# Kernel tuning notes

Hardware: AMD Instinct MI355X
Metric: run time of the kernel (lower is better)

The kernel has to match this reference:

```python
import jax, jax.numpy as jnp
import numpy as np

VOCAB, EMB, HID = 32000, 512, 1024
B, T = 16, 128


def setup_inputs() -> dict:
    key = jax.random.key(0)
    ks = jax.random.split(key, 12)
    bound = 1.0 / np.sqrt(HID)
    u = lambda k, shape: jax.random.uniform(k, shape, jnp.float32, -bound, bound)
    return {
        "sentence": jax.random.randint(ks[0], (B, T), 0, VOCAB),
        "emb": jax.random.normal(ks[1], (VOCAB, EMB), jnp.float32),
        "W_i": u(ks[2], (EMB + HID, HID)), "b_i": u(ks[3], (HID,)),
        "W_f": u(ks[4], (EMB + HID, HID)), "b_f": u(ks[5], (HID,)),
        "W_o": u(ks[6], (EMB + HID, HID)), "b_o": u(ks[7], (HID,)),
        "W_c": u(ks[8], (EMB + HID, HID)), "b_c": u(ks[9], (HID,)),
        "W_hq": u(ks[10], (HID, VOCAB)), "b_q": u(ks[11], (VOCAB,)),
    }


def reference(sentence, emb, W_i, b_i, W_f, b_f, W_o, b_o, W_c, b_c, W_hq, b_q):
    # [B,T,E] -> [T,B,E]
    x = jnp.swapaxes(emb[sentence], 0, 1)
    # Fuse the 4 gate matmuls into one concatenated-weight matmul (same math).
    W = jnp.concatenate([W_i, W_f, W_o, W_c], axis=1)  # [E+H, 4H]
    b = jnp.concatenate([b_i, b_f, b_o, b_c])          # [4H]
    h0 = jnp.zeros((x.shape[1], HID), x.dtype)

    def step(carry, xt):
        h, c = carry
        z = jnp.concatenate([xt, h], axis=1) @ W + b   # [B,4H]
        i, f, o, g = jnp.split(z, 4, axis=1)
        i, f, o = jax.nn.sigmoid(i), jax.nn.sigmoid(f), jax.nn.sigmoid(o)
        c = f * c + i * jnp.tanh(g)
        h = o * jnp.tanh(c)
        return (h, c), h

    _, hs = jax.lax.scan(step, (h0, h0), x)            # [T,B,H]
    out = jnp.einsum('tbh,hv->tbv', hs, W_hq) + b_q    # [T,B,V]
    return jnp.transpose(out, (1, 2, 0))               # [B,V,T] as in torch permute(1,2,0)
```

## Files before the change

kernel.cpp:

```cpp
#include <hip/hip_runtime.h>
#include <math.h>

typedef float f32x4 __attribute__((ext_vector_type(4)));
typedef short bf16x8 __attribute__((ext_vector_type(8)));
typedef unsigned short u16;
typedef unsigned int u32;
typedef unsigned long long u64;

#define FLAG_STRIDE 16
#define ACQ_BASE    8192
#define EPOCH_BASE  8448
#define QCNT_BASE   8512
#define TCNT_BASE   8528
#define FLAG_WORDS  ((TCNT_BASE + 1) * FLAG_STRIDE)
#define NTILE       125

__device__ __forceinline__ u16 f2bf(float f) {
    union { float f; unsigned u; } x; x.f = f;
    unsigned r = x.u + 0x7fff + ((x.u >> 16) & 1);
    return (u16)(r >> 16);
}

__device__ __forceinline__ void gload_lds16(const u16* g, u16* l) {
    __builtin_amdgcn_global_load_lds(
        (const __attribute__((address_space(1))) void*)g,
        (__attribute__((address_space(3))) void*)l, 16, 0, 0);
}

__global__ __launch_bounds__(256) void prep(
    const int* __restrict__ sent, const float* __restrict__ emb, u16* __restrict__ xb,
    const float* __restrict__ bi, const float* __restrict__ bf_,
    const float* __restrict__ bo, const float* __restrict__ bc, float* __restrict__ b4,
    const float* __restrict__ Wi, const float* __restrict__ Wf,
    const float* __restrict__ Wo, const float* __restrict__ Wc, u16* __restrict__ wxt) {
    __shared__ float tile[32][33];
    const int bx = blockIdx.x, tid = threadIdx.x;
    if (bx < 1024) {
        int row = bx * 2 + (tid >> 7);
        int t = row >> 4, b = row & 15;
        int idx = sent[b * 128 + t];
        float4 v = ((const float4*)(emb + (size_t)idx * 512))[tid & 127];
        ushort4 s = { f2bf(v.x), f2bf(v.y), f2bf(v.z), f2bf(v.w) };
        ((ushort4*)(xb + (size_t)row * 512))[tid & 127] = s;
        return;
    }
    if (bx < 1040) {
        int i = (bx - 1024) * 256 + tid;
        const float* p = (i < 1024) ? bi : (i < 2048) ? bf_ : (i < 3072) ? bo : bc;
        b4[i] = p[i & 1023];
        return;
    }
    int q = bx - 1040, g = q >> 9, r = q & 511;
    const float* in = (g == 0) ? Wi : (g == 1) ? Wf : (g == 2) ? Wo : Wc;
    u16* out = wxt + (size_t)g * 1024 * 512;
    int rt = (r >> 5) * 32, ct = (r & 31) * 32;
    {
        int rr = tid >> 3, cq = (tid & 7) * 4;
        float4 v = *(const float4*)(in + (size_t)(rt + rr) * 1024 + ct + cq);
        tile[rr][cq] = v.x; tile[rr][cq + 1] = v.y; tile[rr][cq + 2] = v.z; tile[rr][cq + 3] = v.w;
        __syncthreads();
        int c = tid >> 3, rq = (tid & 7) * 4;
        ushort4 s = { f2bf(tile[rq][c]), f2bf(tile[rq + 1][c]),
                      f2bf(tile[rq + 2][c]), f2bf(tile[rq + 3][c]) };
        *(ushort4*)(out + (size_t)(ct + c) * 512 + rt + rq) = s;
    }
}

__global__ __launch_bounds__(256) void gemm_xz(
    const u16* __restrict__ A, const u16* __restrict__ Bt,
    const float* __restrict__ bias, float* __restrict__ C) {
    const int tid = threadIdx.x;
    const int l = tid & 63, w = tid >> 6;
    const int wr = w >> 1, wc = w & 1;
    const int m0 = blockIdx.x * 128, n0 = blockIdx.y * 128;
    const int K = 512;
    __shared__ __align__(16) u16 As[128 * 64];
    __shared__ __align__(16) u16 Bs[128 * 64];
    f32x4 acc[4][4];
    f32x4 zz = { 0.f, 0.f, 0.f, 0.f };
#pragma unroll
    for (int i = 0; i < 4; i++)
#pragma unroll
        for (int j = 0; j < 4; j++) acc[i][j] = zz;
    for (int kt = 0; kt < (K >> 6); ++kt) {
        __syncthreads();
#pragma unroll
        for (int i = 0; i < 4; i++) {
            int cbase = i * 256 + w * 64;
            int c = cbase + l, row = c >> 3, kc = c & 7;
            gload_lds16(A + (size_t)(m0 + row) * K + kt * 64 + kc * 8, As + (size_t)cbase * 8);
            gload_lds16(Bt + (size_t)(n0 + row) * K + kt * 64 + kc * 8, Bs + (size_t)cbase * 8);
        }
        __syncthreads();
#pragma unroll
        for (int kk = 0; kk < 2; kk++) {
            bf16x8 af[4], bfv[4];
#pragma unroll
            for (int mi = 0; mi < 4; mi++)
                af[mi] = *(const bf16x8*)(As + (wr * 64 + mi * 16 + (l & 15)) * 64 + kk * 32 + (l >> 4) * 8);
#pragma unroll
            for (int ni = 0; ni < 4; ni++)
                bfv[ni] = *(const bf16x8*)(Bs + (wc * 64 + ni * 16 + (l & 15)) * 64 + kk * 32 + (l >> 4) * 8);
#pragma unroll
            for (int mi = 0; mi < 4; mi++)
#pragma unroll
                for (int ni = 0; ni < 4; ni++)
                    acc[mi][ni] = __builtin_amdgcn_mfma_f32_16x16x32_bf16(af[mi], bfv[ni], acc[mi][ni], 0, 0, 0);
        }
    }
    const int lr = l >> 4, lc = l & 15;
#pragma unroll
    for (int ni = 0; ni < 4; ni++) {
        int col = n0 + wc * 64 + ni * 16 + lc;
        float bv = bias[col];
#pragma unroll
        for (int mi = 0; mi < 4; mi++)
#pragma unroll
            for (int r = 0; r < 4; r++) {
                int row = m0 + wr * 64 + mi * 16 + lr * 4 + r;
                C[(size_t)row * 4096 + col] = acc[mi][ni][r] + bv;
            }
    }
}

__global__ __launch_bounds__(512, 2) void lstm_proj(
    u16* __restrict__ hs,
    const float* __restrict__ xz,
    const float* __restrict__ Wi, const float* __restrict__ Wf,
    const float* __restrict__ Wo, const float* __restrict__ Wc,
    u32* __restrict__ flags,
    const float* __restrict__ Whq,
    u16* __restrict__ whqt,
    const float* __restrict__ bq, float* __restrict__ out) {
    __shared__ __align__(16) char smem[98816];
    const int bx = blockIdx.x;
    const int tid = threadIdx.x;
    const int w = tid >> 6, l = tid & 63;

    if (tid == 0)
        __hip_atomic_fetch_add(&flags[(size_t)(ACQ_BASE + (bx & 255)) * FLAG_STRIDE], 0u,
                               __ATOMIC_ACQ_REL, __HIP_MEMORY_SCOPE_AGENT);

    if (bx < 64) {
        u16* hstage = (u16*)smem;
        float (*zlds)[16][17] = (float (*)[16][17])(void*)(smem + 32768);
        u32* lds_cnt = (u32*)(smem + 37632);
        const int j = bx;
        const int row = l & 15, hi = l >> 4;
        if (tid == 0) *lds_cnt = 0;

        bf16x8 wf[32];
        if (w < 4) {
            const float* Wg = (w == 0) ? Wi : (w == 1) ? Wf : (w == 2) ? Wo : Wc;
#pragma unroll
            for (int kk = 0; kk < 32; ++kk)
#pragma unroll
                for (int e = 0; e < 8; ++e)
                    wf[kk][e] = f2bf(Wg[(size_t)(512 + kk * 32 + hi * 8 + e) * 1024 + j * 16 + row]);
        }
        __syncthreads();

        const int b = tid >> 4, hc = tid & 15;
        float cst = 0.f;
        float cz0 = 0.f, cz1 = 0.f, cz2 = 0.f, cz3 = 0.f;
        if (tid < 256) {
            const float* xr0 = xz + (size_t)b * 4096 + j * 16 + hc;
            cz0 = xr0[0]; cz1 = xr0[1024]; cz2 = xr0[2048]; cz3 = xr0[3072];
        }

        for (int t = 0; t < 128; ++t) {
            if (t > 0) {
                const u16* hbase = hs + (size_t)(t - 1) * 16 * 1024;
                {
                    int spins = 0;
                    while (true) {
                        u32 f = 1u;
                        if (l < 8)
                            f = __hip_atomic_load(
                                    &flags[(size_t)((t - 1) * 64 + 8 * w + l) * FLAG_STRIDE],
                                    __ATOMIC_RELAXED, __HIP_MEMORY_SCOPE_SYSTEM);
                        if (__ballot(f != 0u) == ~0ull) break;
                        __builtin_amdgcn_s_sleep(1);
                        if (++spins > (1 << 20)) break;
                    }
                }
#pragma unroll
                for (int q = 0; q < 4; ++q) {
                    int jw0 = 8 * w + 2 * q;
                    gload_lds16(hbase + (size_t)((l & 31) >> 1) * 1024
                                      + (jw0 + (l >> 5)) * 16 + (l & 1) * 8,
                                hstage + (size_t)jw0 * 256);
                }
            }
            float nz0 = 0.f, nz1 = 0.f, nz2 = 0.f, nz3 = 0.f;
            if (t < 127 && tid < 256) {
                const float* xr = xz + (size_t)((t + 1) * 16 + b) * 4096 + j * 16 + hc;
                nz0 = xr[0]; nz1 = xr[1024]; nz2 = xr[2048]; nz3 = xr[3072];
            }
            __syncthreads();
            if (t > 0) {
                if (tid == 0)
                    __hip_atomic_store(&flags[(size_t)(EPOCH_BASE + j) * FLAG_STRIDE], (u32)t,
                                       __ATOMIC_RELAXED, __HIP_MEMORY_SCOPE_SYSTEM);
                if (w < 4) {
                    f32x4 zv = { 0.f, 0.f, 0.f, 0.f };
                    f32x4 ac0 = zv, ac1 = zv, ac2 = zv, ac3 = zv;
#pragma unroll
                    for (int kk = 0; kk < 32; kk += 4) {
#pragma unroll
                        for (int u = 0; u < 4; ++u) {
                            int base = (2 * (kk + u) + (hi >> 1)) * 256 + row * 16 + (hi & 1) * 8;
                            bf16x8 a = *(const bf16x8*)(hstage + base);
                            f32x4& ac = (u == 0) ? ac0 : (u == 1) ? ac1 : (u == 2) ? ac2 : ac3;
                            ac = __builtin_amdgcn_mfma_f32_16x16x32_bf16(a, wf[kk + u], ac, 0, 0, 0);
                        }
                    }
                    f32x4 acc = (ac0 + ac1) + (ac2 + ac3);
#pragma unroll
                    for (int r = 0; r < 4; ++r)
                        zlds[w][hi * 4 + r][row] = acc[r];
                }
            }
            __syncthreads();
            if (tid < 256) {
                float zi = cz0, zf = cz1, zo = cz2, zc = cz3;
                if (t > 0) {
                    zi += zlds[0][b][hc]; zf += zlds[1][b][hc];
                    zo += zlds[2][b][hc]; zc += zlds[3][b][hc];
                }
                float ig = 1.f / (1.f + __expf(-zi));
                float fg = 1.f / (1.f + __expf(-zf));
                float og = 1.f / (1.f + __expf(-zo));
                float gg = tanhf(zc);
                cst = fg * cst + ig * gg;
                float h = og * tanhf(cst);
                float hn = __shfl_xor(h, 1);
                if (!(l & 1)) {
                    unsigned pk = (unsigned)f2bf(h) | ((unsigned)f2bf(hn) << 16);
                    u32* dst = (u32*)hs + (((size_t)(t * 16 + b) * 1024 + j * 16 + hc) >> 1);
                    __hip_atomic_store(dst, pk, __ATOMIC_RELAXED, __HIP_MEMORY_SCOPE_SYSTEM);
                }
                cz0 = nz0; cz1 = nz1; cz2 = nz2; cz3 = nz3;
            }
            if (w < 4) {
                asm volatile("s_waitcnt vmcnt(0)" ::: "memory");
                if (l == 0) {
                    u32 old = atomicAdd(lds_cnt, 1u);
                    if (old == (u32)(4 * t + 3))
                        __hip_atomic_store(&flags[(size_t)(t * 64 + j) * FLAG_STRIDE], 1u,
                                           __ATOMIC_RELAXED, __HIP_MEMORY_SCOPE_SYSTEM);
                }
            }
        }
        if (w == 0) {
            int spins = 0;
            while (true) {
                u32 f = __hip_atomic_load(&flags[(size_t)(127 * 64 + l) * FLAG_STRIDE],
                                          __ATOMIC_RELAXED, __HIP_MEMORY_SCOPE_SYSTEM);
                if (__ballot(f != 0) == ~0ull) break;
                __builtin_amdgcn_s_sleep(1);
                if (++spins > (1 << 20)) break;
            }
            if (l == 0)
                __hip_atomic_store(&flags[(size_t)(EPOCH_BASE + j) * FLAG_STRIDE], 128u,
                                   __ATOMIC_RELAXED, __HIP_MEMORY_SCOPE_SYSTEM);
        }
        return;
    }

    {
        float (*tp)[32][33] = (float (*)[32][33])(void*)smem;
        const int half = tid >> 8, t256 = tid & 255;
        const int r = t256 >> 3, cq = (t256 & 7) * 4;
        const int c = t256 >> 3, rq = (t256 & 7) * 4;
        for (int it = 0; it < 84; ++it) {
            int q = it * 384 + (bx - 64) * 2 + half;
            bool act = q < 32000;
            int rt = 0, ct = 0;
            if (act) { rt = (q / 1000) * 32; ct = (q % 1000) * 32; }
            if (act) {
                float4 v = *(const float4*)(Whq + (size_t)(rt + r) * 32000 + ct + cq);
                tp[half][r][cq] = v.x; tp[half][r][cq + 1] = v.y;
                tp[half][r][cq + 2] = v.z; tp[half][r][cq + 3] = v.w;
            }
            __syncthreads();
            if (act) {
                u64 pk = (u64)f2bf(tp[half][rq][c])
                       | ((u64)f2bf(tp[half][rq + 1][c]) << 16)
                       | ((u64)f2bf(tp[half][rq + 2][c]) << 32)
                       | ((u64)f2bf(tp[half][rq + 3][c]) << 48);
                __hip_atomic_store((u64*)(whqt + (size_t)(ct + c) * 1024 + rt + rq), pk,
                                   __ATOMIC_RELAXED, __HIP_MEMORY_SCOPE_SYSTEM);
            }
            __syncthreads();
        }
        asm volatile("s_waitcnt vmcnt(0)" ::: "memory");
        if (tid == 0)
            __hip_atomic_fetch_add(&flags[(size_t)TCNT_BASE * FLAG_STRIDE], 1u,
                                   __ATOMIC_RELAXED, __HIP_MEMORY_SCOPE_SYSTEM);
    }

    u16* As = (u16*)smem;
    u16* Bs = (u16*)(smem + 32768);
    u32* idx_slot = (u32*)(smem + 98304);
    const int wr = w >> 2, wc = w & 3;
    const int lr = l >> 4, lc = l & 15;

    if (tid == 0)
        *idx_slot = __hip_atomic_fetch_add(&flags[(size_t)QCNT_BASE * FLAG_STRIDE],
                                           1u, __ATOMIC_RELAXED, __HIP_MEMORY_SCOPE_AGENT);
    if (w == 0) {
        int spins = 0;
        while (__hip_atomic_load(&flags[(size_t)TCNT_BASE * FLAG_STRIDE],
                                 __ATOMIC_RELAXED, __HIP_MEMORY_SCOPE_SYSTEM) < 192u) {
            __builtin_amdgcn_s_sleep(8);
            if (++spins > (1 << 20)) break;
        }
    }
    __syncthreads();
    const u32 myIdx = *idx_slot;
    if (myIdx >= NTILE) return;
    const int n0 = (int)myIdx * 256;

    for (int m = 0; m < 16; ++m) {
        if (w == 0) {
            const u32 need = (u32)(8 * m + 8);
            int spins = 0;
            while (__hip_atomic_load(&flags[(size_t)(EPOCH_BASE + (bx & 63)) * FLAG_STRIDE],
                                     __ATOMIC_RELAXED, __HIP_MEMORY_SCOPE_SYSTEM) < need) {
                __builtin_amdgcn_s_sleep(8);
                if (++spins > (1 << 20)) break;
            }
        }
        __syncthreads();

        auto STAGE = [&](int bi, int kt) {
#pragma unroll
            for (int i = 0; i < 2; ++i) {
                int C = i * 512 + tid, r = C >> 3, c = C & 7;
                int sc = c ^ (r & 7);
                int arow = (8 * m + (r & 7)) * 16 + (r >> 3);
                gload_lds16(hs + (size_t)arow * 1024 + kt * 64 + sc * 8,
                            As + (size_t)(bi * 8192 + (i * 512 + w * 64) * 8));
            }
#pragma unroll
            for (int i = 0; i < 4; ++i) {
                int C = i * 512 + tid, r = C >> 3, c = C & 7;
                int sc = c ^ (r & 7);
                gload_lds16(whqt + (size_t)(n0 + r) * 1024 + kt * 64 + sc * 8,
                            Bs + (size_t)(bi * 16384 + (i * 512 + w * 64) * 8));
            }
        };

        f32x4 acc[4][4];
        f32x4 zz = { 0.f, 0.f, 0.f, 0.f };
#pragma unroll
        for (int i = 0; i < 4; i++)
#pragma unroll
            for (int jj = 0; jj < 4; jj++) acc[i][jj] = zz;

        int cur = 0;
        STAGE(0, 0);
        __syncthreads();
        for (int kt = 0; kt < 16; ++kt) {
            if (kt + 1 < 16) STAGE(cur ^ 1, kt + 1);
            const u16* Ab = As + cur * 8192;
            const u16* Bb = Bs + cur * 16384;
#pragma unroll
            for (int kk = 0; kk < 2; ++kk) {
                bf16x8 af[4], bf[4];
#pragma unroll
                for (int mi = 0; mi < 4; ++mi) {
                    int rA = wr * 64 + mi * 16 + lc;
                    int s = (kk * 4 + lr) ^ (rA & 7);
                    af[mi] = *(const bf16x8*)(Ab + rA * 64 + s * 8);
                }
#pragma unroll
                for (int ni = 0; ni < 4; ++ni) {
                    int rB = wc * 64 + ni * 16 + lc;
                    int s = (kk * 4 + lr) ^ (rB & 7);
                    bf[ni] = *(const bf16x8*)(Bb + rB * 64 + s * 8);
                }
#pragma unroll
                for (int mi = 0; mi < 4; ++mi)
#pragma unroll
                    for (int ni = 0; ni < 4; ++ni)
                        acc[mi][ni] = __builtin_amdgcn_mfma_f32_16x16x32_bf16(af[mi], bf[ni], acc[mi][ni], 0, 0, 0);
            }
            __syncthreads();
            cur ^= 1;
        }
#pragma unroll
        for (int ni = 0; ni < 4; ni++) {
            int col = n0 + wc * 64 + ni * 16 + lc;
            float bv = bq[col];
#pragma unroll
            for (int mi = 0; mi < 4; mi++) {
                int r0 = wr * 64 + mi * 16 + lr * 4;
                int bb = r0 >> 3;
                int t0 = 8 * m + (r0 & 7);
                float4 st = { acc[mi][ni][0] + bv, acc[mi][ni][1] + bv,
                              acc[mi][ni][2] + bv, acc[mi][ni][3] + bv };
                *(float4*)(out + (size_t)bb * 4096000 + (size_t)col * 128 + t0) = st;
            }
        }
    }
}

extern "C" void kernel_launch(void* const* d_in, const int* in_sizes, int n_in,
                              void* d_out, int out_size, void* d_ws, size_t ws_size,
                              hipStream_t stream) {
    const int*   sent = (const int*)d_in[0];
    const float* emb  = (const float*)d_in[1];
    const float* W_i  = (const float*)d_in[2];
    const float* b_i  = (const float*)d_in[3];
    const float* W_f  = (const float*)d_in[4];
    const float* b_f  = (const float*)d_in[5];
    const float* W_o  = (const float*)d_in[6];
    const float* b_o  = (const float*)d_in[7];
    const float* W_c  = (const float*)d_in[8];
    const float* b_c  = (const float*)d_in[9];
    const float* W_hq = (const float*)d_in[10];
    const float* b_q  = (const float*)d_in[11];
    float* out = (float*)d_out;

    char* ws = (char*)d_ws;
    size_t off = 0;
    auto alloc = [&](size_t bytes) { void* p = ws + off; off += (bytes + 255) & ~255ull; return p; };
    u32*   flags = (u32*)alloc((size_t)FLAG_WORDS * 4);
    float* b4   = (float*)alloc((size_t)4096 * 4);
    u16*   xb   = (u16*)alloc((size_t)2048 * 512 * 2);
    u16*   wxt  = (u16*)alloc((size_t)4096 * 512 * 2);
    u16*   hs   = (u16*)alloc((size_t)2048 * 1024 * 2);
    float* xz   = (float*)alloc((size_t)2048 * 4096 * 4);
    u16*   whqt = (u16*)alloc((size_t)32000 * 1024 * 2);

    hipMemsetAsync(flags, 0, (size_t)FLAG_WORDS * 4, stream);
    prep<<<3088, 256, 0, stream>>>(sent, emb, xb, b_i, b_f, b_o, b_c, b4,
                                   W_i, W_f, W_o, W_c, wxt);
    gemm_xz<<<dim3(16, 32), 256, 0, stream>>>(xb, wxt, b4, xz);
    lstm_proj<<<256, 512, 0, stream>>>(hs, xz, W_i, W_f, W_o, W_c,
                                       flags, W_hq, whqt, b_q, out);
}
```

Baseline: 657.0 us.

## Fuse input projection into recurrent LSTM kernel, drop separate xz GEMM

```diff
diff --git a/kernel.cpp b/kernel.cpp
--- a/kernel.cpp
+++ b/kernel.cpp
@@ -28,111 +28,28 @@
 }
 
 __global__ __launch_bounds__(256) void prep(
-    const int* __restrict__ sent, const float* __restrict__ emb, u16* __restrict__ xb,
-    const float* __restrict__ bi, const float* __restrict__ bf_,
-    const float* __restrict__ bo, const float* __restrict__ bc, float* __restrict__ b4,
-    const float* __restrict__ Wi, const float* __restrict__ Wf,
-    const float* __restrict__ Wo, const float* __restrict__ Wc, u16* __restrict__ wxt) {
-    __shared__ float tile[32][33];
+    const int* __restrict__ sent, const float* __restrict__ emb, u16* __restrict__ xb) {
     const int bx = blockIdx.x, tid = threadIdx.x;
-    if (bx < 1024) {
-        int row = bx * 2 + (tid >> 7);
-        int t = row >> 4, b = row & 15;
-        int idx = sent[b * 128 + t];
-        float4 v = ((const float4*)(emb + (size_t)idx * 512))[tid & 127];
-        ushort4 s = { f2bf(v.x), f2bf(v.y), f2bf(v.z), f2bf(v.w) };
-        ((ushort4*)(xb + (size_t)row * 512))[tid & 127] = s;
-        return;
-    }
-    if (bx < 1040) {
-        int i = (bx - 1024) * 256 + tid;
-        const float* p = (i < 1024) ? bi : (i < 2048) ? bf_ : (i < 3072) ? bo : bc;
-        b4[i] = p[i & 1023];
-        return;
-    }
-    int q = bx - 1040, g = q >> 9, r = q & 511;
-    const float* in = (g == 0) ? Wi : (g == 1) ? Wf : (g == 2) ? Wo : Wc;
-    u16* out = wxt + (size_t)g * 1024 * 512;
-    int rt = (r >> 5) * 32, ct = (r & 31) * 32;
-    {
-        int rr = tid >> 3, cq = (tid & 7) * 4;
-        float4 v = *(const float4*)(in + (size_t)(rt + rr) * 1024 + ct + cq);
-        tile[rr][cq] = v.x; tile[rr][cq + 1] = v.y; tile[rr][cq + 2] = v.z; tile[rr][cq + 3] = v.w;
-        __syncthreads();
-        int c = tid >> 3, rq = (tid & 7) * 4;
-        ushort4 s = { f2bf(tile[rq][c]), f2bf(tile[rq + 1][c]),
-                      f2bf(tile[rq + 2][c]), f2bf(tile[rq + 3][c]) };
-        *(ushort4*)(out + (size_t)(ct + c) * 512 + rt + rq) = s;
-    }
-}
-
-__global__ __launch_bounds__(256) void gemm_xz(
-    const u16* __restrict__ A, const u16* __restrict__ Bt,
-    const float* __restrict__ bias, float* __restrict__ C) {
-    const int tid = threadIdx.x;
-    const int l = tid & 63, w = tid >> 6;
-    const int wr = w >> 1, wc = w & 1;
-    const int m0 = blockIdx.x * 128, n0 = blockIdx.y * 128;
-    const int K = 512;
-    __shared__ __align__(16) u16 As[128 * 64];
-    __shared__ __align__(16) u16 Bs[128 * 64];
-    f32x4 acc[4][4];
-    f32x4 zz = { 0.f, 0.f, 0.f, 0.f };
-#pragma unroll
-    for (int i = 0; i < 4; i++)
-#pragma unroll
-        for (int j = 0; j < 4; j++) acc[i][j] = zz;
-    for (int kt = 0; kt < (K >> 6); ++kt) {
-        __syncthreads();
-#pragma unroll
-        for (int i = 0; i < 4; i++) {
-            int cbase = i * 256 + w * 64;
-            int c = cbase + l, row = c >> 3, kc = c & 7;
-            gload_lds16(A + (size_t)(m0 + row) * K + kt * 64 + kc * 8, As + (size_t)cbase * 8);
-            gload_lds16(Bt + (size_t)(n0 + row) * K + kt * 64 + kc * 8, Bs + (size_t)cbase * 8);
-        }
-        __syncthreads();
-#pragma unroll
-        for (int kk = 0; kk < 2; kk++) {
-            bf16x8 af[4], bfv[4];
-#pragma unroll
-            for (int mi = 0; mi < 4; mi++)
-                af[mi] = *(const bf16x8*)(As + (wr * 64 + mi * 16 + (l & 15)) * 64 + kk * 32 + (l >> 4) * 8);
-#pragma unroll
-            for (int ni = 0; ni < 4; ni++)
-                bfv[ni] = *(const bf16x8*)(Bs + (wc * 64 + ni * 16 + (l & 15)) * 64 + kk * 32 + (l >> 4) * 8);
-#pragma unroll
-            for (int mi = 0; mi < 4; mi++)
-#pragma unroll
-                for (int ni = 0; ni < 4; ni++)
-                    acc[mi][ni] = __builtin_amdgcn_mfma_f32_16x16x32_bf16(af[mi], bfv[ni], acc[mi][ni], 0, 0, 0);
-        }
-    }
-    const int lr = l >> 4, lc = l & 15;
-#pragma unroll
-    for (int ni = 0; ni < 4; ni++) {
-        int col = n0 + wc * 64 + ni * 16 + lc;
-        float bv = bias[col];
-#pragma unroll
-        for (int mi = 0; mi < 4; mi++)
-#pragma unroll
-            for (int r = 0; r < 4; r++) {
-                int row = m0 + wr * 64 + mi * 16 + lr * 4 + r;
-                C[(size_t)row * 4096 + col] = acc[mi][ni][r] + bv;
-            }
-    }
+    int row = bx * 2 + (tid >> 7);
+    int t = row >> 4, b = row & 15;
+    int idx = sent[b * 128 + t];
+    float4 v = ((const float4*)(emb + (size_t)idx * 512))[tid & 127];
+    ushort4 s = { f2bf(v.x), f2bf(v.y), f2bf(v.z), f2bf(v.w) };
+    ((ushort4*)(xb + (size_t)row * 512))[tid & 127] = s;
 }
 
 __global__ __launch_bounds__(512, 2) void lstm_proj(
     u16* __restrict__ hs,
-    const float* __restrict__ xz,
+    const u16* __restrict__ xb,
     const float* __restrict__ Wi, const float* __restrict__ Wf,
     const float* __restrict__ Wo, const float* __restrict__ Wc,
+    const float* __restrict__ bi, const float* __restrict__ bf_,
+    const float* __restrict__ bo, const float* __restrict__ bc,
     u32* __restrict__ flags,
     const float* __restrict__ Whq,
     u16* __restrict__ whqt,
     const float* __restrict__ bq, float* __restrict__ out) {
-    __shared__ __align__(16) char smem[98816];
+    __shared__ __align__(16) char smem[135680];
     const int bx = blockIdx.x;
     const int tid = threadIdx.x;
     const int w = tid >> 6, l = tid & 63;
@@ -143,8 +60,10 @@
 
     if (bx < 64) {
         u16* hstage = (u16*)smem;
-        float (*zlds)[16][17] = (float (*)[16][17])(void*)(smem + 32768);
-        u32* lds_cnt = (u32*)(smem + 37632);
+        u16* xstage = (u16*)(smem + 32768);
+        u16* wfx    = (u16*)(smem + 65536);
+        float (*zlds)[16][17] = (float (*)[16][17])(void*)(smem + 131072);
+        u32* lds_cnt = (u32*)(smem + 135424);
         const int j = bx;
         const int row = l & 15, hi = l >> 4;
         if (tid == 0) *lds_cnt = 0;
@@ -157,18 +76,42 @@
 #pragma unroll
                 for (int e = 0; e < 8; ++e)
                     wf[kk][e] = f2bf(Wg[(size_t)(512 + kk * 32 + hi * 8 + e) * 1024 + j * 16 + row]);
+#pragma unroll
+            for (int kk = 0; kk < 16; ++kk) {
+                bf16x8 v;
+#pragma unroll
+                for (int e = 0; e < 8; ++e)
+                    v[e] = f2bf(Wg[(size_t)(kk * 32 + hi * 8 + e) * 1024 + j * 16 + row]);
+                *(bf16x8*)(wfx + ((size_t)(w * 16 + kk) * 64 + l) * 8) = v;
+            }
+        }
+        float bzi = 0.f, bzf = 0.f, bzo = 0.f, bzc = 0.f;
+        const int b = tid >> 4, hc = tid & 15;
+        if (tid < 256) {
+            bzi = bi[j * 16 + hc]; bzf = bf_[j * 16 + hc];
+            bzo = bo[j * 16 + hc]; bzc = bc[j * 16 + hc];
+        }
+#pragma unroll
+        for (int q = 0; q < 2; ++q) {
+            int jx0 = (w * 2 + q) * 2;
+            gload_lds16(xb + (size_t)((l & 31) >> 1) * 512 + (jx0 + (l >> 5)) * 16 + (l & 1) * 8,
+                        xstage + (size_t)jx0 * 256);
         }
         __syncthreads();
 
-        const int b = tid >> 4, hc = tid & 15;
         float cst = 0.f;
-        float cz0 = 0.f, cz1 = 0.f, cz2 = 0.f, cz3 = 0.f;
-        if (tid < 256) {
-            const float* xr0 = xz + (size_t)b * 4096 + j * 16 + hc;
-            cz0 = xr0[0]; cz1 = xr0[1024]; cz2 = xr0[2048]; cz3 = xr0[3072];
-        }
 
         for (int t = 0; t < 128; ++t) {
+            if (t < 127) {
+                const u16* xbase = xb + (size_t)(t + 1) * 16 * 512;
+                u16* xd = xstage + ((t + 1) & 1) * 8192;
+#pragma unroll
+                for (int q = 0; q < 2; ++q) {
+                    int jx0 = (w * 2 + q) * 2;
+                    gload_lds16(xbase + (size_t)((l & 31) >> 1) * 512 + (jx0 + (l >> 5)) * 16 + (l & 1) * 8,
+                                xd + (size_t)jx0 * 256);
+                }
+            }
             if (t > 0) {
                 const u16* hbase = hs + (size_t)(t - 1) * 16 * 1024;
                 {
@@ -192,27 +135,38 @@
                                 hstage + (size_t)jw0 * 256);
                 }
             }
-            float nz0 = 0.f, nz1 = 0.f, nz2 = 0.f, nz3 = 0.f;
-            if (t < 127 && tid < 256) {
-                const float* xr = xz + (size_t)((t + 1) * 16 + b) * 4096 + j * 16 + hc;
-                nz0 = xr[0]; nz1 = xr[1024]; nz2 = xr[2048]; nz3 = xr[3072];
-            }
-            __syncthreads();
-            if (t > 0) {
-                if (tid == 0)
+            __syncthreads();
+            {
+                if (t > 0 && tid == 0)
                     __hip_atomic_store(&flags[(size_t)(EPOCH_BASE + j) * FLAG_STRIDE], (u32)t,
                                        __ATOMIC_RELAXED, __HIP_MEMORY_SCOPE_SYSTEM);
                 if (w < 4) {
+                    const u16* xs = xstage + (t & 1) * 8192;
                     f32x4 zv = { 0.f, 0.f, 0.f, 0.f };
                     f32x4 ac0 = zv, ac1 = zv, ac2 = zv, ac3 = zv;
 #pragma unroll
-                    for (int kk = 0; kk < 32; kk += 4) {
+                    for (int kk = 0; kk < 16; kk += 4) {
 #pragma unroll
                         for (int u = 0; u < 4; ++u) {
-                            int base = (2 * (kk + u) + (hi >> 1)) * 256 + row * 16 + (hi & 1) * 8;
-                            bf16x8 a = *(const bf16x8*)(hstage + base);
+                            int c = kk + u;
+                            bf16x8 a = *(const bf16x8*)(xs + (2 * c + (hi >> 1)) * 256
+                                                        + row * 16 + (hi & 1) * 8);
+                            bf16x8 bx = *(const bf16x8*)(wfx + ((size_t)(w * 16 + c) * 64 + l) * 8);
                             f32x4& ac = (u == 0) ? ac0 : (u == 1) ? ac1 : (u == 2) ? ac2 : ac3;
-                            ac = __builtin_amdgcn_mfma_f32_16x16x32_bf16(a, wf[kk + u], ac, 0, 0, 0);
+                            ac = __builtin_amdgcn_mfma_f32_16x16x32_bf16(a, bx, ac, 0, 0, 0);
+                        }
+                    }
+                    if (t > 0) {
+#pragma unroll
+                        for (int kk = 0; kk < 32; kk += 4) {
+#pragma unroll
+                            for (int u = 0; u < 4; ++u) {
+                                int c = kk + u;
+                                int base = (2 * c + (hi >> 1)) * 256 + row * 16 + (hi & 1) * 8;
+                                bf16x8 a = *(const bf16x8*)(hstage + base);
+                                f32x4& ac = (u == 0) ? ac0 : (u == 1) ? ac1 : (u == 2) ? ac2 : ac3;
+                                ac = __builtin_amdgcn_mfma_f32_16x16x32_bf16(a, wf[c], ac, 0, 0, 0);
+                            }
                         }
                     }
                     f32x4 acc = (ac0 + ac1) + (ac2 + ac3);
@@ -223,11 +177,10 @@
             }
             __syncthreads();
             if (tid < 256) {
-                float zi = cz0, zf = cz1, zo = cz2, zc = cz3;
-                if (t > 0) {
-                    zi += zlds[0][b][hc]; zf += zlds[1][b][hc];
-                    zo += zlds[2][b][hc]; zc += zlds[3][b][hc];
-                }
+                float zi = zlds[0][b][hc] + bzi;
+                float zf = zlds[1][b][hc] + bzf;
+                float zo = zlds[2][b][hc] + bzo;
+                float zc = zlds[3][b][hc] + bzc;
                 float ig = 1.f / (1.f + __expf(-zi));
                 float fg = 1.f / (1.f + __expf(-zf));
                 float og = 1.f / (1.f + __expf(-zo));
@@ -240,7 +193,6 @@
                     u32* dst = (u32*)hs + (((size_t)(t * 16 + b) * 1024 + j * 16 + hc) >> 1);
                     __hip_atomic_store(dst, pk, __ATOMIC_RELAXED, __HIP_MEMORY_SCOPE_SYSTEM);
                 }
-                cz0 = nz0; cz1 = nz1; cz2 = nz2; cz3 = nz3;
             }
             if (w < 4) {
                 asm volatile("s_waitcnt vmcnt(0)" ::: "memory");
@@ -428,17 +380,13 @@
     size_t off = 0;
     auto alloc = [&](size_t bytes) { void* p = ws + off; off += (bytes + 255) & ~255ull; return p; };
     u32*   flags = (u32*)alloc((size_t)FLAG_WORDS * 4);
-    float* b4   = (float*)alloc((size_t)4096 * 4);
     u16*   xb   = (u16*)alloc((size_t)2048 * 512 * 2);
-    u16*   wxt  = (u16*)alloc((size_t)4096 * 512 * 2);
     u16*   hs   = (u16*)alloc((size_t)2048 * 1024 * 2);
-    float* xz   = (float*)alloc((size_t)2048 * 4096 * 4);
     u16*   whqt = (u16*)alloc((size_t)32000 * 1024 * 2);
 
     hipMemsetAsync(flags, 0, (size_t)FLAG_WORDS * 4, stream);
-    prep<<<3088, 256, 0, stream>>>(sent, emb, xb, b_i, b_f, b_o, b_c, b4,
-                                   W_i, W_f, W_o, W_c, wxt);
-    gemm_xz<<<dim3(16, 32), 256, 0, stream>>>(xb, wxt, b4, xz);
-    lstm_proj<<<256, 512, 0, stream>>>(hs, xz, W_i, W_f, W_o, W_c,
+    prep<<<1024, 256, 0, stream>>>(sent, emb, xb);
+    lstm_proj<<<256, 512, 0, stream>>>(hs, xb, W_i, W_f, W_o, W_c,
+                                       b_i, b_f, b_o, b_c,
                                        flags, W_hq, whqt, b_q, out);
 }
```

After: 649.0 us. About the same (-1.2%).
